# Performance work log

Hardware: AMD Instinct MI355X
Metric: run time of the kernel (lower is better)

The kernel has to match this reference:

```python
import jax, jax.numpy as jnp
import numpy as np

B, CIN, CMID, COUT, H, W = 4, 64, 128, 128, 128, 128
K = 9  # 3x3 taps
EPS = 1e-5


def conv3x3(x, w, b):
    # standard 3x3 conv, stride 1, pad 1, NCHW / OIHW
    y = jax.lax.conv_general_dilated(x, w, (1, 1), ((1, 1), (1, 1)),
                                     dimension_numbers=('NCHW', 'OIHW', 'NCHW'))
    return y + b[None, :, None, None]


def deform_conv3x3(x, offset, w, b):
    # torchvision DeformConv2d semantics (v1, no mask), kernel 3, pad 1, stride 1.
    # offset: [B, 2*K, H, W] with per-tap (dy, dx) pairs.
    Bn, C, Hn, Wn = x.shape
    off = offset.reshape(Bn, K, 2, Hn, Wn)
    off_y, off_x = off[:, :, 0], off[:, :, 1]          # [B,K,H,W]
    ky = (jnp.arange(K) // 3).astype(x.dtype)          # tap row 0..2
    kx = (jnp.arange(K) % 3).astype(x.dtype)           # tap col 0..2
    # sampling positions: p = out_pos - pad + tap + offset
    py = jnp.arange(Hn, dtype=x.dtype)[None, None, :, None] - 1.0 + ky[None, :, None, None] + off_y
    px = jnp.arange(Wn, dtype=x.dtype)[None, None, None, :] - 1.0 + kx[None, :, None, None] + off_x
    y0 = jnp.floor(py); x0 = jnp.floor(px)
    wy1 = py - y0; wx1 = px - x0                       # bilinear fractions
    y0i = y0.astype(jnp.int32); x0i = x0.astype(jnp.int32)
    xf = x.reshape(Bn, C, Hn * Wn)

    def gather(iy, ix):
        valid = ((iy >= 0) & (iy < Hn) & (ix >= 0) & (ix < Wn)).astype(x.dtype)
        idx = jnp.clip(iy, 0, Hn - 1) * Wn + jnp.clip(ix, 0, Wn - 1)  # [B,K,H,W]
        g = jax.vmap(lambda xb, ib: xb[:, ib])(xf, idx)               # [B,C,K,H,W]
        return g, valid

    g00, v00 = gather(y0i, x0i)
    g01, v01 = gather(y0i, x0i + 1)
    g10, v10 = gather(y0i + 1, x0i)
    g11, v11 = gather(y0i + 1, x0i + 1)

    def wmul(g, v, wgt):
        return g * (v * wgt)[:, None]                  # broadcast over channel dim

    sampled = (wmul(g00, v00, (1 - wy1) * (1 - wx1)) +
               wmul(g01, v01, (1 - wy1) * wx1) +
               wmul(g10, v10, wy1 * (1 - wx1)) +
               wmul(g11, v11, wy1 * wx1))              # [B,C,K,H,W]
    out = jnp.einsum('bckhw,ock->bohw', sampled, w.reshape(w.shape[0], C, K))
    return out + b[None, :, None, None]


def batchnorm_relu(x, gamma, beta):
    # training-mode BN: batch statistics over (N,H,W), biased variance
    mean = jnp.mean(x, axis=(0, 2, 3), keepdims=True)
    var = jnp.mean(jnp.square(x - mean), axis=(0, 2, 3), keepdims=True)
    y = (x - mean) * jax.lax.rsqrt(var + EPS)
    return jax.nn.relu(y * gamma[None, :, None, None] + beta[None, :, None, None])


def setup_inputs() -> dict:
    key = jax.random.key(0)
    ks = jax.random.split(key, 13)
    s = 0.05  # small weights keep offsets small / sampling mostly in-bounds
    return {
        'x': jax.random.normal(ks[0], (B, CIN, H, W), jnp.float32),
        'w_off1': jax.random.normal(ks[1], (2 * K, CIN, 3, 3), jnp.float32) * s,
        'b_off1': jnp.zeros((2 * K,), jnp.float32),
        'w1': jax.random.normal(ks[2], (CMID, CIN, 3, 3), jnp.float32) * s,
        'b1': jax.random.normal(ks[3], (CMID,), jnp.float32) * s,
        'g1': jnp.ones((CMID,), jnp.float32),
        'be1': jnp.zeros((CMID,), jnp.float32),
        'w_off2': jax.random.normal(ks[4], (2 * K, CMID, 3, 3), jnp.float32) * s,
        'b_off2': jnp.zeros((2 * K,), jnp.float32),
        'w2': jax.random.normal(ks[5], (COUT, CMID, 3, 3), jnp.float32) * s,
        'b2': jax.random.normal(ks[6], (COUT,), jnp.float32) * s,
        'g2': jnp.ones((COUT,), jnp.float32),
        'be2': jnp.zeros((COUT,), jnp.float32),
    }


def reference(x, w_off1, b_off1, w1, b1, g1, be1, w_off2, b_off2, w2, b2, g2, be2):
    offset1 = conv3x3(x, w_off1, b_off1)
    out = deform_conv3x3(x, offset1, w1, b1)
    out = batchnorm_relu(out, g1, be1)
    offset2 = conv3x3(out, w_off2, b_off2)
    out = deform_conv3x3(out, offset2, w2, b2)
    out = batchnorm_relu(out, g2, be2)
    return out
```

## Files before the change

kernel.cpp:

```cpp
#include <hip/hip_runtime.h>
#include <hip/hip_bf16.h>

#define BB 4
#define H_ 128
#define W_ 128
#define HWP 16384
#define CIN1 64
#define CMID 128
#define KOFF 18

typedef short short8 __attribute__((ext_vector_type(8)));
typedef float floatx4 __attribute__((ext_vector_type(4)));

#define WS_AB   16
#define WS_CVT  288
#define CVT_TOTAL 4447396
#define WS_WF1  4447744
#define WS_WF2  4484608
#define WS_XT   4558336
#define WS_OFF  6655488
#define WS_Y1   7835136
#define WS_Y1T  16223744
#define WS_PART 21600000
#define WS_Y2   WS_Y1

#define R_X     0
#define R_WOFF1 4194304
#define R_BOFF1 4204672
#define R_W1    4204690
#define R_B1    4278418
#define R_G1    4278546
#define R_BE1   4278674
#define R_WOFF2 4278802
#define R_BOFF2 4299538
#define R_W2    4299556
#define R_B2    4447012
#define R_G2    4447140
#define R_BE2   4447268

struct SrcPtrs { const void* p[13]; };

__device__ inline short f2bf(float f) {
    __hip_bfloat16 h = __float2bfloat16(f);
    return *reinterpret_cast<short*>(&h);
}
__device__ inline float bf2f(unsigned short u) {
    return __uint_as_float(((unsigned int)u) << 16);
}
__device__ inline float bfu_lo(unsigned int u) { return __uint_as_float(u << 16); }
__device__ inline float bfu_hi(unsigned int u) { return __uint_as_float(u & 0xFFFF0000u); }
__device__ inline float rl_f(float v, int i) {
    return __int_as_float(__builtin_amdgcn_readlane(__float_as_int(v), i));
}

__global__ void probe_dtype_k(const unsigned int* __restrict__ g1, int* __restrict__ flag) {
    if (threadIdx.x == 0 && blockIdx.x == 0) {
        flag[0] = ((g1[0] & 0xFFFFu) != 0u) ? 1 : 0;
    }
}

__global__ __launch_bounds__(256) void convert_inputs_k(SrcPtrs sp, float* __restrict__ dst,
                                                        const int* __restrict__ flag, int total) {
    int i = blockIdx.x * 256 + threadIdx.x;
    if (i >= total) return;
    constexpr int prefix[13] = {0, R_WOFF1, R_BOFF1, R_W1, R_B1, R_G1, R_BE1,
                                R_WOFF2, R_BOFF2, R_W2, R_B2, R_G2, R_BE2};
    const void* src = sp.p[0];
    int base = 0;
#pragma unroll
    for (int q = 1; q < 13; ++q) {
        if (i >= prefix[q]) { src = sp.p[q]; base = prefix[q]; }
    }
    int local = i - base;
    float v;
    if (flag[0] != 0) {
        v = bf2f(((const unsigned short*)src)[local]);
    } else {
        v = ((const float*)src)[local];
    }
    dst[i] = v;
}

template <int CIN>
__global__ __launch_bounds__(256) void wf_build_k(const float* __restrict__ w, short* __restrict__ wf) {
    constexpr int KSTEPS = CIN * 9 / 32;
    int idx = blockIdx.x * 256 + threadIdx.x;
    int j    = idx & 7;
    int lane = (idx >> 3) & 63;
    int rem  = idx >> 9;
    int ks   = rem % KSTEPS;
    int ct   = rem / KSTEPS;
    int co = ct * 16 + (lane & 15);
    int k  = ks * 32 + (lane >> 4) * 8 + j;
    int ci = k & (CIN - 1);
    int kk = k / CIN;
    wf[idx] = f2bf(w[(co * CIN + ci) * 9 + kk]);
}

__global__ __launch_bounds__(256) void xt_build_k(const float* __restrict__ x, unsigned short* __restrict__ xt) {
    __shared__ __align__(4) short s_t[64 * 66];
    int bi  = blockIdx.x;
    int hw0 = (bi & 255) * 64;
    int b   = bi >> 8;
    int t   = threadIdx.x;
    int hwp = t & 63;
#pragma unroll
    for (int it = 0; it < 16; ++it) {
        int c = it * 4 + (t >> 6);
        float v = x[((long)(b * 64 + c) << 14) + hw0 + hwp];
        s_t[hwp * 66 + c] = f2bf(v);
    }
    __syncthreads();
#pragma unroll
    for (int it = 0; it < 8; ++it) {
        int i  = it * 256 + t;
        int c2 = (i & 31) * 2;
        int hw2 = i >> 5;
        int sv = *(const int*)&s_t[hw2 * 66 + c2];
        *(int*)&xt[((long)((b << 14) + hw0 + hw2)) * 64 + c2] = sv;
    }
}

template <int CIN>
__global__ __launch_bounds__(256) void conv3x3_atomic_k(const float* __restrict__ x,
                                                        const float* __restrict__ w,
                                                        const float* __restrict__ bias,
                                                        float* __restrict__ outp) {
    constexpr int CIQ = CIN / 4;
    int bi = blockIdx.x;
    int h  = bi & 127;
    int b  = (bi >> 7) & 3;
    int q  = bi >> 9;
    int t  = threadIdx.x;
    int wq = t & 127;
    int cg = __builtin_amdgcn_readfirstlane(t >> 7);
    int co0 = cg * 9;
    int ci0 = q * CIQ;

    float acc[9];
#pragma unroll
    for (int j = 0; j < 9; ++j) acc[j] = (q == 0) ? bias[co0 + j] : 0.f;

    const float* xb = x + ((long)(b * CIN + ci0) << 14);
    bool bm = h > 0, bp = h < H_ - 1, bl = wq > 0, br = wq < W_ - 1;
    int rm = (bm ? h - 1 : 0) << 7;
    int rc = h << 7;
    int rp = (bp ? h + 1 : H_ - 1) << 7;

#pragma unroll 2
    for (int ci = 0; ci < CIQ; ++ci) {
        const float* plane = xb + ((long)ci << 14);
        float v0 = plane[rm + wq - 1], v1 = plane[rm + wq], v2 = plane[rm + wq + 1];
        float v3 = plane[rc + wq - 1], v4 = plane[rc + wq], v5 = plane[rc + wq + 1];
        float v6 = plane[rp + wq - 1], v7 = plane[rp + wq], v8 = plane[rp + wq + 1];
        v0 = (bm && bl) ? v0 : 0.f;
        v1 = bm ? v1 : 0.f;
        v2 = (bm && br) ? v2 : 0.f;
        v3 = bl ? v3 : 0.f;
        v5 = br ? v5 : 0.f;
        v6 = (bp && bl) ? v6 : 0.f;
        v7 = bp ? v7 : 0.f;
        v8 = (bp && br) ? v8 : 0.f;
#pragma unroll
        for (int j = 0; j < 9; ++j) {
            const float* wk = w + ((long)(co0 + j) * CIN + ci0 + ci) * 9;
            acc[j] += v0 * wk[0] + v1 * wk[1] + v2 * wk[2]
                    + v3 * wk[3] + v4 * wk[4] + v5 * wk[5]
                    + v6 * wk[6] + v7 * wk[7] + v8 * wk[8];
        }
    }

    long ob = ((long)(b * KOFF + co0) << 14) + (h << 7) + wq;
#pragma unroll
    for (int j = 0; j < 9; ++j) atomicAdd(&outp[ob + ((long)j << 14)], acc[j]);
}

template <int CIN>
__device__ inline void build_table(const float* __restrict__ off, int b, int h, int w0,
                                   int lane, int wv,
                                   int& tpk, float& tw0, float& tw1, float& tw2, float& tw3) {
    tpk = 0; tw0 = tw1 = tw2 = tw3 = 0.f;
    if (lane < 36) {
        int r = wv + 4 * lane;
        int p = r & 15;
        int k = r >> 4;
        int wpix = w0 + p;
        long obase = ((long)(b * KOFF) << 14) + (h << 7) + wpix;
        float oy = off[obase + ((long)(2 * k) << 14)];
        float ox = off[obase + ((long)(2 * k + 1) << 14)];
        float py = (float)(h - 1 + (k / 3)) + oy;
        float px = (float)(wpix - 1 + (k % 3)) + ox;
        float fy = floorf(py), fx = floorf(px);
        float wy = py - fy, wx = px - fx;
        int y0 = (int)fy, x0 = (int)fx;
        int y1 = y0 + 1, x1 = x0 + 1;
        bool vy0 = (y0 >= 0) && (y0 < H_);
        bool vy1 = (y1 >= 0) && (y1 < H_);
        bool vx0 = (x0 >= 0) && (x0 < W_);
        bool vx1 = (x1 >= 0) && (x1 < W_);
        float wy0 = 1.f - wy, wx0 = 1.f - wx;
        tw0 = (vy0 && vx0) ? wy0 * wx0 : 0.f;
        tw1 = (vy0 && vx1) ? wy0 * wx  : 0.f;
        tw2 = (vy1 && vx0) ? wy  * wx0 : 0.f;
        tw3 = (vy1 && vx1) ? wy  * wx  : 0.f;
        int iy0 = min(max(y0, 0), H_ - 1), iy1 = min(max(y1, 0), H_ - 1);
        int ix0 = min(max(x0, 0), W_ - 1), ix1 = min(max(x1, 0), W_ - 1);
        int dx = ix1 - ix0;
        int dy = iy1 - iy0;
        tpk = (iy0 * W_ + ix0) | (dx << 14) | (dy << 15);
    }
}

template <int NB>
__device__ inline void gather_batch128(const unsigned short* __restrict__ xb, short* __restrict__ s_samp,
                                       int PADc, int i0, int kkbase, int wv, int lane,
                                       int tpk, float tw0, float tw1, float tw2, float tw3) {
    uint4 ub[NB];
#pragma unroll
    for (int j = 0; j < NB; ++j) {
        int pk = __builtin_amdgcn_readlane(tpk, i0 + j);
        const unsigned short* b00 = xb + (pk & 0x3FFF) * 128;
        const unsigned short* b01 = b00 + ((pk >> 14) & 1) * 128;
        const unsigned short* b10 = b00 + ((pk >> 15) & 1) * (W_ * 128);
        const unsigned short* b11 = b01 + ((pk >> 15) & 1) * (W_ * 128);
        ub[j].x = *(const unsigned int*)(b00 + 2 * lane);
        ub[j].y = *(const unsigned int*)(b01 + 2 * lane);
        ub[j].z = *(const unsigned int*)(b10 + 2 * lane);
        ub[j].w = *(const unsigned int*)(b11 + 2 * lane);
    }
#pragma unroll
    for (int j = 0; j < NB; ++j) {
        int i = i0 + j;
        int r = wv + 4 * i;
        float w00 = rl_f(tw0, i), w01 = rl_f(tw1, i), w10 = rl_f(tw2, i), w11 = rl_f(tw3, i);
        float vlo = w00 * bfu_lo(ub[j].x) + w01 * bfu_lo(ub[j].y)
                  + w10 * bfu_lo(ub[j].z) + w11 * bfu_lo(ub[j].w);
        float vhi = w00 * bfu_hi(ub[j].x) + w01 * bfu_hi(ub[j].y)
                  + w10 * bfu_hi(ub[j].z) + w11 * bfu_hi(ub[j].w);
        __hip_bfloat162 h2 = __float22bfloat162_rn(make_float2(vlo, vhi));
        *(unsigned int*)&s_samp[(r & 15) * PADc + ((r >> 4) - kkbase) * 128 + 2 * lane] =
            *reinterpret_cast<unsigned int*>(&h2);
    }
}

template <int NB>
__device__ inline void gather_batch64(const unsigned short* __restrict__ xb, short* __restrict__ s_samp,
                                      int PADc, int i0, int wv, int lane,
                                      int tpk, float tw0, float tw1, float tw2, float tw3) {
    unsigned short q0[NB], q1[NB], q2[NB], q3[NB];
#pragma unroll
    for (int j = 0; j < NB; ++j) {
        int pk = __builtin_amdgcn_readlane(tpk, i0 + j);
        const unsigned short* b00 = xb + (pk & 0x3FFF) * 64;
        const unsigned short* b01 = b00 + ((pk >> 14) & 1) * 64;
        const unsigned short* b10 = b00 + ((pk >> 15) & 1) * (W_ * 64);
        const unsigned short* b11 = b01 + ((pk >> 15) & 1) * (W_ * 64);
        q0[j] = b00[lane]; q1[j] = b01[lane]; q2[j] = b10[lane]; q3[j] = b11[lane];
    }
#pragma unroll
    for (int j = 0; j < NB; ++j) {
        int i = i0 + j;
        int r = wv + 4 * i;
        float w00 = rl_f(tw0, i), w01 = rl_f(tw1, i), w10 = rl_f(tw2, i), w11 = rl_f(tw3, i);
        float v = w00 * bf2f(q0[j]) + w01 * bf2f(q1[j]) + w10 * bf2f(q2[j]) + w11 * bf2f(q3[j]);
        s_samp[(r & 15) * PADc + (r >> 4) * 64 + lane] = f2bf(v);
    }
}

__global__ __launch_bounds__(256, 6) void deform_mfma64_k(const unsigned short* __restrict__ xt,
                                                          const float* __restrict__ off,
                                                          const short* __restrict__ wf,
                                                          const float* __restrict__ bias,
                                                          float* __restrict__ out) {
    constexpr int CIN = 64;
    constexpr int K = 576;
    constexpr int PADc = K + 8;
    constexpr int KSTEPS = K / 32;
    __shared__ __align__(16) short s_samp[16 * PADc];

    int bi = blockIdx.x;
    int w0 = (bi & 7) * 16;
    int h  = (bi >> 3) & 127;
    int b  = bi >> 10;
    int t  = threadIdx.x;
    int lane = t & 63;
    int wv   = t >> 6;

    int tpk; float tw0, tw1, tw2, tw3;
    build_table<CIN>(off, b, h, w0, lane, wv, tpk, tw0, tw1, tw2, tw3);
    const unsigned short* xb = xt + (long)b * HWP * CIN;

    gather_batch64<12>(xb, s_samp, PADc,  0, wv, lane, tpk, tw0, tw1, tw2, tw3);
    gather_batch64<12>(xb, s_samp, PADc, 12, wv, lane, tpk, tw0, tw1, tw2, tw3);
    gather_batch64<12>(xb, s_samp, PADc, 24, wv, lane, tpk, tw0, tw1, tw2, tw3);
    __syncthreads();

    int p_   = lane & 15;
    int quad = lane >> 4;
    int ct0 = wv * 2, ct1 = wv * 2 + 1;
    floatx4 acc0, acc1;
#pragma unroll
    for (int r = 0; r < 4; ++r) {
        acc0[r] = bias[ct0 * 16 + quad * 4 + r];
        acc1[r] = bias[ct1 * 16 + quad * 4 + r];
    }
#pragma unroll 3
    for (int ks = 0; ks < KSTEPS; ++ks) {
        short8 bfrag = *(const short8*)&s_samp[p_ * PADc + ks * 32 + quad * 8];
        short8 a0 = *(const short8*)&wf[(((long)ct0 * KSTEPS + ks) * 64 + lane) * 8];
        short8 a1 = *(const short8*)&wf[(((long)ct1 * KSTEPS + ks) * 64 + lane) * 8];
        acc0 = __builtin_amdgcn_mfma_f32_16x16x32_bf16(a0, bfrag, acc0, 0, 0, 0);
        acc1 = __builtin_amdgcn_mfma_f32_16x16x32_bf16(a1, bfrag, acc1, 0, 0, 0);
    }

    long ob = ((long)(b * 128) << 14) + (h << 7) + w0 + p_;
#pragma unroll
    for (int r = 0; r < 4; ++r) {
        out[ob + ((long)(ct0 * 16 + quad * 4 + r) << 14)] = acc0[r];
        out[ob + ((long)(ct1 * 16 + quad * 4 + r) << 14)] = acc1[r];
    }
}

__global__ __launch_bounds__(256, 6) void deform_mfma128_k(const unsigned short* __restrict__ xt,
                                                           const float* __restrict__ off,
                                                           const short* __restrict__ wf,
                                                           const float* __restrict__ bias,
                                                           float* __restrict__ out) {
    constexpr int KSTEPS = 36;
    constexpr int PADc = 5 * 128 + 8;
    __shared__ __align__(16) short s_samp[16 * PADc];

    int bi = blockIdx.x;
    int w0 = (bi & 7) * 16;
    int h  = (bi >> 3) & 127;
    int b  = bi >> 10;
    int t  = threadIdx.x;
    int lane = t & 63;
    int wv   = t >> 6;

    int tpk; float tw0, tw1, tw2, tw3;
    build_table<128>(off, b, h, w0, lane, wv, tpk, tw0, tw1, tw2, tw3);
    const unsigned short* xb = xt + (long)b * HWP * 128;

    int p_   = lane & 15;
    int quad = lane >> 4;
    int ct0 = wv * 2, ct1 = wv * 2 + 1;
    floatx4 acc0, acc1;
#pragma unroll
    for (int r = 0; r < 4; ++r) {
        acc0[r] = bias[ct0 * 16 + quad * 4 + r];
        acc1[r] = bias[ct1 * 16 + quad * 4 + r];
    }

    gather_batch128<8>(xb, s_samp, PADc, 0, 0, wv, lane, tpk, tw0, tw1, tw2, tw3);
    gather_batch128<8>(xb, s_samp, PADc, 8, 0, wv, lane, tpk, tw0, tw1, tw2, tw3);
    __syncthreads();
#pragma unroll 4
    for (int ks = 0; ks < 16; ++ks) {
        short8 bfrag = *(const short8*)&s_samp[p_ * PADc + ks * 32 + quad * 8];
        short8 a0 = *(const short8*)&wf[(((long)ct0 * KSTEPS + ks) * 64 + lane) * 8];
        short8 a1 = *(const short8*)&wf[(((long)ct1 * KSTEPS + ks) * 64 + lane) * 8];
        acc0 = __builtin_amdgcn_mfma_f32_16x16x32_bf16(a0, bfrag, acc0, 0, 0, 0);
        acc1 = __builtin_amdgcn_mfma_f32_16x16x32_bf16(a1, bfrag, acc1, 0, 0, 0);
    }
    __syncthreads();

    gather_batch128<10>(xb, s_samp, PADc, 16, 4, wv, lane, tpk, tw0, tw1, tw2, tw3);
    gather_batch128<10>(xb, s_samp, PADc, 26, 4, wv, lane, tpk, tw0, tw1, tw2, tw3);
    __syncthreads();
#pragma unroll 4
    for (int ks = 16; ks < 36; ++ks) {
        short8 bfrag = *(const short8*)&s_samp[p_ * PADc + (ks - 16) * 32 + quad * 8];
        short8 a0 = *(const short8*)&wf[(((long)ct0 * KSTEPS + ks) * 64 + lane) * 8];
        short8 a1 = *(const short8*)&wf[(((long)ct1 * KSTEPS + ks) * 64 + lane) * 8];
        acc0 = __builtin_amdgcn_mfma_f32_16x16x32_bf16(a0, bfrag, acc0, 0, 0, 0);
        acc1 = __builtin_amdgcn_mfma_f32_16x16x32_bf16(a1, bfrag, acc1, 0, 0, 0);
    }

    long ob = ((long)(b * 128) << 14) + (h << 7) + w0 + p_;
#pragma unroll
    for (int r = 0; r < 4; ++r) {
        out[ob + ((long)(ct0 * 16 + quad * 4 + r) << 14)] = acc0[r];
        out[ob + ((long)(ct1 * 16 + quad * 4 + r) << 14)] = acc1[r];
    }
}

__global__ __launch_bounds__(256) void bn_stats_part_k(const float* __restrict__ y, float* __restrict__ part) {
    int bi = blockIdx.x;
    int c = bi & 127;
    int b = bi >> 7;
    int t = threadIdx.x;
    const float4* p4 = (const float4*)(y + ((long)(b * 128 + c) << 14));
    float sum = 0.f, ss = 0.f;
#pragma unroll
    for (int i = 0; i < 16; ++i) {
        float4 v = p4[t + 256 * i];
        sum += v.x + v.y + v.z + v.w;
        ss  += v.x * v.x + v.y * v.y + v.z * v.z + v.w * v.w;
    }
#pragma unroll
    for (int o = 32; o > 0; o >>= 1) { sum += __shfl_down(sum, o); ss += __shfl_down(ss, o); }
    __shared__ float s1[4], s2[4];
    int wave = t >> 6;
    if ((t & 63) == 0) { s1[wave] = sum; s2[wave] = ss; }
    __syncthreads();
    if (t == 0) {
        part[bi]       = s1[0] + s1[1] + s1[2] + s1[3];
        part[512 + bi] = s2[0] + s2[1] + s2[2] + s2[3];
    }
}

__global__ __launch_bounds__(256) void bn_apply_dual_k(float* __restrict__ y, const float* __restrict__ part,
                                                       const float* __restrict__ g, const float* __restrict__ be,
                                                       unsigned short* __restrict__ yt) {
    __shared__ __align__(4) short s_t[64 * 134];
    __shared__ float s_a[128], s_sh[128];
    int t = threadIdx.x;
    if (t < 128) {
        float sum = part[t] + part[128 + t] + part[256 + t] + part[384 + t];
        float ss  = part[512 + t] + part[640 + t] + part[768 + t] + part[896 + t];
        float mean = sum * (1.f / 65536.f);
        float var  = ss  * (1.f / 65536.f) - mean * mean;
        float inv  = rsqrtf(var + 1e-5f);
        float a = g[t] * inv;
        s_a[t]  = a;
        s_sh[t] = be[t] - mean * a;
    }
    __syncthreads();

    int bi  = blockIdx.x;
    int hw0 = (bi & 255) * 64;
    int b   = bi >> 8;
    int hwp = t & 63;
#pragma unroll 4
    for (int it = 0; it < 32; ++it) {
        int c = it * 4 + (t >> 6);
        float a = s_a[c], sh = s_sh[c];
        long addr = ((long)(b * 128 + c) << 14) + hw0 + hwp;
        float v = y[addr];
        v = fmaxf(v * a + sh, 0.f);
        y[addr] = v;
        s_t[hwp * 134 + c] = f2bf(v);
    }
    __syncthreads();
#pragma unroll 4
    for (int it = 0; it < 16; ++it) {
        int i   = it * 256 + t;
        int c2  = (i & 63) * 2;
        int hw2 = i >> 6;
        int sv = *(const int*)&s_t[hw2 * 134 + c2];
        *(int*)&yt[((long)((b << 14) + hw0 + hw2)) * 128 + c2] = sv;
    }
}

__global__ __launch_bounds__(256) void bn_apply_out_k(const float* __restrict__ y, const float* __restrict__ part,
                                                      const float* __restrict__ g, const float* __restrict__ be,
                                                      const int* __restrict__ flag, void* __restrict__ out, int total4) {
    __shared__ float s_a[128], s_sh[128];
    int t = threadIdx.x;
    if (t < 128) {
        float sum = part[t] + part[128 + t] + part[256 + t] + part[384 + t];
        float ss  = part[512 + t] + part[640 + t] + part[768 + t] + part[896 + t];
        float mean = sum * (1.f / 65536.f);
        float var  = ss  * (1.f / 65536.f) - mean * mean;
        float inv  = rsqrtf(var + 1e-5f);
        float a = g[t] * inv;
        s_a[t]  = a;
        s_sh[t] = be[t] - mean * a;
    }
    __syncthreads();

    int i = blockIdx.x * 256 + t;
    if (i >= total4) return;
    int c = (i >> 12) & 127;
    float a = s_a[c], sh = s_sh[c];
    float4 v = reinterpret_cast<const float4*>(y)[i];
    v.x = fmaxf(v.x * a + sh, 0.f);
    v.y = fmaxf(v.y * a + sh, 0.f);
    v.z = fmaxf(v.z * a + sh, 0.f);
    v.w = fmaxf(v.w * a + sh, 0.f);
    if (flag[0] != 0) {
        ushort4 u;
        u.x = (unsigned short)f2bf(v.x);
        u.y = (unsigned short)f2bf(v.y);
        u.z = (unsigned short)f2bf(v.z);
        u.w = (unsigned short)f2bf(v.w);
        reinterpret_cast<ushort4*>(out)[i] = u;
    } else {
        reinterpret_cast<float4*>(out)[i] = v;
    }
}

extern "C" void kernel_launch(void* const* d_in, const int* in_sizes, int n_in,
                              void* d_out, int out_size, void* d_ws, size_t ws_size,
                              hipStream_t stream) {
    float* ws   = (float*)d_ws;
    int*   flag = (int*)d_ws;
    float* cvt  = ws + WS_CVT;

    const float* X     = cvt + R_X;
    const float* Woff1 = cvt + R_WOFF1;
    const float* Boff1 = cvt + R_BOFF1;
    const float* W1f   = cvt + R_W1;
    const float* B1f   = cvt + R_B1;
    const float* G1    = cvt + R_G1;
    const float* Be1   = cvt + R_BE1;
    const float* Woff2 = cvt + R_WOFF2;
    const float* Boff2 = cvt + R_BOFF2;
    const float* W2f   = cvt + R_W2;
    const float* B2f   = cvt + R_B2;
    const float* G2    = cvt + R_G2;
    const float* Be2   = cvt + R_BE2;

    short* WF1 = (short*)(ws + WS_WF1);
    short* WF2 = (short*)(ws + WS_WF2);
    unsigned short* XT  = (unsigned short*)(ws + WS_XT);
    unsigned short* Y1T = (unsigned short*)(ws + WS_Y1T);
    float* OFF  = ws + WS_OFF;
    float* PART = ws + WS_PART;
    float* Y1   = ws + WS_Y1;
    float* Y2   = ws + WS_Y2;

    SrcPtrs sp;
    for (int j = 0; j < 13; ++j) sp.p[j] = d_in[j];

    probe_dtype_k<<<1, 64, 0, stream>>>((const unsigned int*)d_in[5], flag);
    convert_inputs_k<<<(CVT_TOTAL + 255) / 256, 256, 0, stream>>>(sp, cvt, flag, CVT_TOTAL);
    wf_build_k<64><<<288, 256, 0, stream>>>(W1f, WF1);
    wf_build_k<128><<<576, 256, 0, stream>>>(W2f, WF2);
    xt_build_k<<<1024, 256, 0, stream>>>(X, XT);

    hipMemsetAsync(OFF, 0, (size_t)KOFF * 65536 * 4, stream);
    conv3x3_atomic_k<64><<<BB * 128 * 4, 256, 0, stream>>>(X, Woff1, Boff1, OFF);
    deform_mfma64_k<<<BB * 128 * 8, 256, 0, stream>>>(XT, OFF, WF1, B1f, Y1);
    bn_stats_part_k<<<512, 256, 0, stream>>>(Y1, PART);
    bn_apply_dual_k<<<1024, 256, 0, stream>>>(Y1, PART, G1, Be1, Y1T);

    hipMemsetAsync(OFF, 0, (size_t)KOFF * 65536 * 4, stream);
    conv3x3_atomic_k<128><<<BB * 128 * 4, 256, 0, stream>>>(Y1, Woff2, Boff2, OFF);
    deform_mfma128_k<<<BB * 128 * 8, 256, 0, stream>>>(Y1T, OFF, WF2, B2f, Y2);
    bn_stats_part_k<<<512, 256, 0, stream>>>(Y2, PART);
    bn_apply_out_k<<<(BB * 128 * HWP / 4 + 255) / 256, 256, 0, stream>>>(Y2, PART, G2, Be2, flag, d_out, BB * 128 * HWP / 4);
}
```

Measured before the change: 354.0 us.

## Replace atomic offset conv with two-part split; widen deform tiles to 32 pixels

The offset conv now splits input channels into two halves that each write to their own buffer (OFF and OFFB), and the deformable kernels add the two halves together. This removes the memset and the atomic adds. The deformable MFMA kernels now use 512-thread blocks over 32-pixel tiles, with each wave owning one output-channel tile. Each weight fragment is reused for two pixel subtiles instead of loading two weight fragments per step. The 64-channel gather now uses 32-bit loads with half-wave pairing. The trade-off is a larger LDS footprint and fewer blocks per CU, and the offset conv grid has half as many blocks.

```diff
diff --git a/kernel.cpp b/kernel.cpp
--- a/kernel.cpp
+++ b/kernel.cpp
@@ -21,6 +21,7 @@
 #define WS_OFF  6655488
 #define WS_Y1   7835136
 #define WS_Y1T  16223744
+#define WS_OFFB 20418048
 #define WS_PART 21600000
 #define WS_Y2   WS_Y1
 
@@ -122,11 +123,12 @@
 }
 
 template <int CIN>
-__global__ __launch_bounds__(256) void conv3x3_atomic_k(const float* __restrict__ x,
-                                                        const float* __restrict__ w,
-                                                        const float* __restrict__ bias,
-                                                        float* __restrict__ outp) {
-    constexpr int CIQ = CIN / 4;
+__global__ __launch_bounds__(256) void conv3x3_part_k(const float* __restrict__ x,
+                                                      const float* __restrict__ w,
+                                                      const float* __restrict__ bias,
+                                                      float* __restrict__ outp,
+                                                      float* __restrict__ outpb) {
+    constexpr int CIQ = CIN / 2;
     int bi = blockIdx.x;
     int h  = bi & 127;
     int b  = (bi >> 7) & 3;
@@ -170,24 +172,26 @@
         }
     }
 
+    float* o = (q == 0) ? outp : outpb;
     long ob = ((long)(b * KOFF + co0) << 14) + (h << 7) + wq;
 #pragma unroll
-    for (int j = 0; j < 9; ++j) atomicAdd(&outp[ob + ((long)j << 14)], acc[j]);
-}
-
-template <int CIN>
-__device__ inline void build_table(const float* __restrict__ off, int b, int h, int w0,
-                                   int lane, int wv,
-                                   int& tpk, float& tw0, float& tw1, float& tw2, float& tw3) {
+    for (int j = 0; j < 9; ++j) o[ob + ((long)j << 14)] = acc[j];
+}
+
+__device__ inline void build_table2(const float* __restrict__ off, const float* __restrict__ offb,
+                                    int b, int h, int w0, int lane, int wv,
+                                    int& tpk, float& tw0, float& tw1, float& tw2, float& tw3) {
     tpk = 0; tw0 = tw1 = tw2 = tw3 = 0.f;
     if (lane < 36) {
-        int r = wv + 4 * lane;
-        int p = r & 15;
-        int k = r >> 4;
+        int r = wv + 8 * lane;
+        int p = r & 31;
+        int k = r >> 5;
         int wpix = w0 + p;
         long obase = ((long)(b * KOFF) << 14) + (h << 7) + wpix;
-        float oy = off[obase + ((long)(2 * k) << 14)];
-        float ox = off[obase + ((long)(2 * k + 1) << 14)];
+        long oyi = obase + ((long)(2 * k) << 14);
+        long oxi = obase + ((long)(2 * k + 1) << 14);
+        float oy = off[oyi] + offb[oyi];
+        float ox = off[oxi] + offb[oxi];
         float py = (float)(h - 1 + (k / 3)) + oy;
         float px = (float)(wpix - 1 + (k % 3)) + ox;
         float fy = floorf(py), fx = floorf(px);
@@ -212,9 +216,10 @@
 }
 
 template <int NB>
-__device__ inline void gather_batch128(const unsigned short* __restrict__ xb, short* __restrict__ s_samp,
-                                       int PADc, int i0, int kkbase, int wv, int lane,
-                                       int tpk, float tw0, float tw1, float tw2, float tw3) {
+__device__ inline void gather_batch128v2(const unsigned short* __restrict__ xb, short* __restrict__ s_samp,
+                                         int i0, int kkbase, int wv, int lane,
+                                         int tpk, float tw0, float tw1, float tw2, float tw3) {
+    constexpr int PADc = 648;
     uint4 ub[NB];
 #pragma unroll
     for (int j = 0; j < NB; ++j) {
@@ -231,157 +236,179 @@
 #pragma unroll
     for (int j = 0; j < NB; ++j) {
         int i = i0 + j;
-        int r = wv + 4 * i;
+        int r = wv + 8 * i;
         float w00 = rl_f(tw0, i), w01 = rl_f(tw1, i), w10 = rl_f(tw2, i), w11 = rl_f(tw3, i);
         float vlo = w00 * bfu_lo(ub[j].x) + w01 * bfu_lo(ub[j].y)
                   + w10 * bfu_lo(ub[j].z) + w11 * bfu_lo(ub[j].w);
         float vhi = w00 * bfu_hi(ub[j].x) + w01 * bfu_hi(ub[j].y)
                   + w10 * bfu_hi(ub[j].z) + w11 * bfu_hi(ub[j].w);
         __hip_bfloat162 h2 = __float22bfloat162_rn(make_float2(vlo, vhi));
-        *(unsigned int*)&s_samp[(r & 15) * PADc + ((r >> 4) - kkbase) * 128 + 2 * lane] =
+        *(unsigned int*)&s_samp[(r & 31) * PADc + ((r >> 5) - kkbase) * 128 + 2 * lane] =
             *reinterpret_cast<unsigned int*>(&h2);
     }
 }
 
-template <int NB>
-__device__ inline void gather_batch64(const unsigned short* __restrict__ xb, short* __restrict__ s_samp,
-                                      int PADc, int i0, int wv, int lane,
-                                      int tpk, float tw0, float tw1, float tw2, float tw3) {
-    unsigned short q0[NB], q1[NB], q2[NB], q3[NB];
-#pragma unroll
-    for (int j = 0; j < NB; ++j) {
-        int pk = __builtin_amdgcn_readlane(tpk, i0 + j);
+template <int NBP>
+__device__ inline void gather_batch64v2(const unsigned short* __restrict__ xb, short* __restrict__ s_samp,
+                                        int i0, int wv, int half, int li,
+                                        int tpk, float tw0, float tw1, float tw2, float tw3) {
+    constexpr int PADc = 584;
+    uint4 ub[NBP];
+#pragma unroll
+    for (int j = 0; j < NBP; ++j) {
+        int iA = i0 + 2 * j, iB = iA + 1;
+        int pkA = __builtin_amdgcn_readlane(tpk, iA);
+        int pkB = __builtin_amdgcn_readlane(tpk, iB);
+        int pk = half ? pkB : pkA;
         const unsigned short* b00 = xb + (pk & 0x3FFF) * 64;
         const unsigned short* b01 = b00 + ((pk >> 14) & 1) * 64;
         const unsigned short* b10 = b00 + ((pk >> 15) & 1) * (W_ * 64);
         const unsigned short* b11 = b01 + ((pk >> 15) & 1) * (W_ * 64);
-        q0[j] = b00[lane]; q1[j] = b01[lane]; q2[j] = b10[lane]; q3[j] = b11[lane];
-    }
-#pragma unroll
-    for (int j = 0; j < NB; ++j) {
-        int i = i0 + j;
-        int r = wv + 4 * i;
-        float w00 = rl_f(tw0, i), w01 = rl_f(tw1, i), w10 = rl_f(tw2, i), w11 = rl_f(tw3, i);
-        float v = w00 * bf2f(q0[j]) + w01 * bf2f(q1[j]) + w10 * bf2f(q2[j]) + w11 * bf2f(q3[j]);
-        s_samp[(r & 15) * PADc + (r >> 4) * 64 + lane] = f2bf(v);
-    }
-}
-
-__global__ __launch_bounds__(256, 6) void deform_mfma64_k(const unsigned short* __restrict__ xt,
+        ub[j].x = *(const unsigned int*)(b00 + 2 * li);
+        ub[j].y = *(const unsigned int*)(b01 + 2 * li);
+        ub[j].z = *(const unsigned int*)(b10 + 2 * li);
+        ub[j].w = *(const unsigned int*)(b11 + 2 * li);
+    }
+#pragma unroll
+    for (int j = 0; j < NBP; ++j) {
+        int iA = i0 + 2 * j, iB = iA + 1;
+        float w00 = half ? rl_f(tw0, iB) : rl_f(tw0, iA);
+        float w01 = half ? rl_f(tw1, iB) : rl_f(tw1, iA);
+        float w10 = half ? rl_f(tw2, iB) : rl_f(tw2, iA);
+        float w11 = half ? rl_f(tw3, iB) : rl_f(tw3, iA);
+        float vlo = w00 * bfu_lo(ub[j].x) + w01 * bfu_lo(ub[j].y)
+                  + w10 * bfu_lo(ub[j].z) + w11 * bfu_lo(ub[j].w);
+        float vhi = w00 * bfu_hi(ub[j].x) + w01 * bfu_hi(ub[j].y)
+                  + w10 * bfu_hi(ub[j].z) + w11 * bfu_hi(ub[j].w);
+        __hip_bfloat162 h2 = __float22bfloat162_rn(make_float2(vlo, vhi));
+        int r = wv + 8 * (half ? iB : iA);
+        *(unsigned int*)&s_samp[(r & 31) * PADc + (r >> 5) * 64 + 2 * li] =
+            *reinterpret_cast<unsigned int*>(&h2);
+    }
+}
+
+__global__ __launch_bounds__(512, 4) void deform_mfma64_k(const unsigned short* __restrict__ xt,
                                                           const float* __restrict__ off,
+                                                          const float* __restrict__ offb,
                                                           const short* __restrict__ wf,
                                                           const float* __restrict__ bias,
                                                           float* __restrict__ out) {
-    constexpr int CIN = 64;
-    constexpr int K = 576;
-    constexpr int PADc = K + 8;
-    constexpr int KSTEPS = K / 32;
-    __shared__ __align__(16) short s_samp[16 * PADc];
+    constexpr int KSTEPS = 18;
+    constexpr int PADc = 584;
+    __shared__ __align__(16) short s_samp[32 * PADc];
 
     int bi = blockIdx.x;
-    int w0 = (bi & 7) * 16;
-    int h  = (bi >> 3) & 127;
-    int b  = bi >> 10;
+    int w0 = (bi & 3) * 32;
+    int h  = (bi >> 2) & 127;
+    int b  = bi >> 9;
     int t  = threadIdx.x;
     int lane = t & 63;
     int wv   = t >> 6;
 
     int tpk; float tw0, tw1, tw2, tw3;
-    build_table<CIN>(off, b, h, w0, lane, wv, tpk, tw0, tw1, tw2, tw3);
-    const unsigned short* xb = xt + (long)b * HWP * CIN;
-
-    gather_batch64<12>(xb, s_samp, PADc,  0, wv, lane, tpk, tw0, tw1, tw2, tw3);
-    gather_batch64<12>(xb, s_samp, PADc, 12, wv, lane, tpk, tw0, tw1, tw2, tw3);
-    gather_batch64<12>(xb, s_samp, PADc, 24, wv, lane, tpk, tw0, tw1, tw2, tw3);
+    build_table2(off, offb, b, h, w0, lane, wv, tpk, tw0, tw1, tw2, tw3);
+    const unsigned short* xb = xt + (long)b * HWP * 64;
+    int half = lane >> 5, li = lane & 31;
+
+    gather_batch64v2<6>(xb, s_samp,  0, wv, half, li, tpk, tw0, tw1, tw2, tw3);
+    gather_batch64v2<6>(xb, s_samp, 12, wv, half, li, tpk, tw0, tw1, tw2, tw3);
+    gather_batch64v2<6>(xb, s_samp, 24, wv, half, li, tpk, tw0, tw1, tw2, tw3);
     __syncthreads();
 
     int p_   = lane & 15;
     int quad = lane >> 4;
-    int ct0 = wv * 2, ct1 = wv * 2 + 1;
+    int ct = wv;
     floatx4 acc0, acc1;
 #pragma unroll
     for (int r = 0; r < 4; ++r) {
-        acc0[r] = bias[ct0 * 16 + quad * 4 + r];
-        acc1[r] = bias[ct1 * 16 + quad * 4 + r];
+        float bv = bias[ct * 16 + quad * 4 + r];
+        acc0[r] = bv;
+        acc1[r] = bv;
     }
 #pragma unroll 3
     for (int ks = 0; ks < KSTEPS; ++ks) {
-        short8 bfrag = *(const short8*)&s_samp[p_ * PADc + ks * 32 + quad * 8];
-        short8 a0 = *(const short8*)&wf[(((long)ct0 * KSTEPS + ks) * 64 + lane) * 8];
-        short8 a1 = *(const short8*)&wf[(((long)ct1 * KSTEPS + ks) * 64 + lane) * 8];
-        acc0 = __builtin_amdgcn_mfma_f32_16x16x32_bf16(a0, bfrag, acc0, 0, 0, 0);
-        acc1 = __builtin_amdgcn_mfma_f32_16x16x32_bf16(a1, bfrag, acc1, 0, 0, 0);
+        short8 a  = *(const short8*)&wf[(((long)ct * KSTEPS + ks) * 64 + lane) * 8];
+        short8 b0 = *(const short8*)&s_samp[p_ * PADc + ks * 32 + quad * 8];
+        short8 b1 = *(const short8*)&s_samp[(16 + p_) * PADc + ks * 32 + quad * 8];
+        acc0 = __builtin_amdgcn_mfma_f32_16x16x32_bf16(a, b0, acc0, 0, 0, 0);
+        acc1 = __builtin_amdgcn_mfma_f32_16x16x32_bf16(a, b1, acc1, 0, 0, 0);
     }
 
     long ob = ((long)(b * 128) << 14) + (h << 7) + w0 + p_;
 #pragma unroll
     for (int r = 0; r < 4; ++r) {
-        out[ob + ((long)(ct0 * 16 + quad * 4 + r) << 14)] = acc0[r];
-        out[ob + ((long)(ct1 * 16 + quad * 4 + r) << 14)] = acc1[r];
-    }
-}
-
-__global__ __launch_bounds__(256, 6) void deform_mfma128_k(const unsigned short* __restrict__ xt,
+        long cpl = (long)(ct * 16 + quad * 4 + r) << 14;
+        out[ob + cpl]      = acc0[r];
+        out[ob + 16 + cpl] = acc1[r];
+    }
+}
+
+__global__ __launch_bounds__(512, 4) void deform_mfma128_k(const unsigned short* __restrict__ xt,
                                                            const float* __restrict__ off,
+                                                           const float* __restrict__ offb,
                                                            const short* __restrict__ wf,
                                                            const float* __restrict__ bias,
                                                            float* __restrict__ out) {
     constexpr int KSTEPS = 36;
-    constexpr int PADc = 5 * 128 + 8;
-    __shared__ __align__(16) short s_samp[16 * PADc];
+    constexpr int PADc = 648;
+    __shared__ __align__(16) short s_samp[32 * PADc];
 
     int bi = blockIdx.x;
-    int w0 = (bi & 7) * 16;
-    int h  = (bi >> 3) & 127;
-    int b  = bi >> 10;
+    int w0 = (bi & 3) * 32;
+    int h  = (bi >> 2) & 127;
+    int b  = bi >> 9;
     int t  = threadIdx.x;
     int lane = t & 63;
     int wv   = t >> 6;
 
     int tpk; float tw0, tw1, tw2, tw3;
-    build_table<128>(off, b, h, w0, lane, wv, tpk, tw0, tw1, tw2, tw3);
+    build_table2(off, offb, b, h, w0, lane, wv, tpk, tw0, tw1, tw2, tw3);
     const unsigned short* xb = xt + (long)b * HWP * 128;
 
     int p_   = lane & 15;
     int quad = lane >> 4;
-    int ct0 = wv * 2, ct1 = wv * 2 + 1;
+    int ct = wv;
     floatx4 acc0, acc1;
 #pragma unroll
     for (int r = 0; r < 4; ++r) {
-        acc0[r] = bias[ct0 * 16 + quad * 4 + r];
-        acc1[r] = bias[ct1 * 16 + quad * 4 + r];
-    }
-
-    gather_batch128<8>(xb, s_samp, PADc, 0, 0, wv, lane, tpk, tw0, tw1, tw2, tw3);
-    gather_batch128<8>(xb, s_samp, PADc, 8, 0, wv, lane, tpk, tw0, tw1, tw2, tw3);
+        float bv = bias[ct * 16 + quad * 4 + r];
+        acc0[r] = bv;
+        acc1[r] = bv;
+    }
+
+    gather_batch128v2<8>(xb, s_samp, 0, 0, wv, lane, tpk, tw0, tw1, tw2, tw3);
+    gather_batch128v2<8>(xb, s_samp, 8, 0, wv, lane, tpk, tw0, tw1, tw2, tw3);
     __syncthreads();
 #pragma unroll 4
     for (int ks = 0; ks < 16; ++ks) {
-        short8 bfrag = *(const short8*)&s_samp[p_ * PADc + ks * 32 + quad * 8];
-        short8 a0 = *(const short8*)&wf[(((long)ct0 * KSTEPS + ks) * 64 + lane) * 8];
-        short8 a1 = *(const short8*)&wf[(((long)ct1 * KSTEPS + ks) * 64 + lane) * 8];
-        acc0 = __builtin_amdgcn_mfma_f32_16x16x32_bf16(a0, bfrag, acc0, 0, 0, 0);
-        acc1 = __builtin_amdgcn_mfma_f32_16x16x32_bf16(a1, bfrag, acc1, 0, 0, 0);
-    }
-    __syncthreads();
-
-    gather_batch128<10>(xb, s_samp, PADc, 16, 4, wv, lane, tpk, tw0, tw1, tw2, tw3);
-    gather_batch128<10>(xb, s_samp, PADc, 26, 4, wv, lane, tpk, tw0, tw1, tw2, tw3);
+        short8 a  = *(const short8*)&wf[(((long)ct * KSTEPS + ks) * 64 + lane) * 8];
+        short8 b0 = *(const short8*)&s_samp[p_ * PADc + ks * 32 + quad * 8];
+        short8 b1 = *(const short8*)&s_samp[(16 + p_) * PADc + ks * 32 + quad * 8];
+        acc0 = __builtin_amdgcn_mfma_f32_16x16x32_bf16(a, b0, acc0, 0, 0, 0);
+        acc1 = __builtin_amdgcn_mfma_f32_16x16x32_bf16(a, b1, acc1, 0, 0, 0);
+    }
+    __syncthreads();
+
+    gather_batch128v2<5>(xb, s_samp, 16, 4, wv, lane, tpk, tw0, tw1, tw2, tw3);
+    gather_batch128v2<5>(xb, s_samp, 21, 4, wv, lane, tpk, tw0, tw1, tw2, tw3);
+    gather_batch128v2<5>(xb, s_samp, 26, 4, wv, lane, tpk, tw0, tw1, tw2, tw3);
+    gather_batch128v2<5>(xb, s_samp, 31, 4, wv, lane, tpk, tw0, tw1, tw2, tw3);
     __syncthreads();
 #pragma unroll 4
-    for (int ks = 16; ks < 36; ++ks) {
-        short8 bfrag = *(const short8*)&s_samp[p_ * PADc + (ks - 16) * 32 + quad * 8];
-        short8 a0 = *(const short8*)&wf[(((long)ct0 * KSTEPS + ks) * 64 + lane) * 8];
-        short8 a1 = *(const short8*)&wf[(((long)ct1 * KSTEPS + ks) * 64 + lane) * 8];
-        acc0 = __builtin_amdgcn_mfma_f32_16x16x32_bf16(a0, bfrag, acc0, 0, 0, 0);
-        acc1 = __builtin_amdgcn_mfma_f32_16x16x32_bf16(a1, bfrag, acc1, 0, 0, 0);
+    for (int ks = 16; ks < KSTEPS; ++ks) {
+        short8 a  = *(const short8*)&wf[(((long)ct * KSTEPS + ks) * 64 + lane) * 8];
+        short8 b0 = *(const short8*)&s_samp[p_ * PADc + (ks - 16) * 32 + quad * 8];
+        short8 b1 = *(const short8*)&s_samp[(16 + p_) * PADc + (ks - 16) * 32 + quad * 8];
+        acc0 = __builtin_amdgcn_mfma_f32_16x16x32_bf16(a, b0, acc0, 0, 0, 0);
+        acc1 = __builtin_amdgcn_mfma_f32_16x16x32_bf16(a, b1, acc1, 0, 0, 0);
     }
 
     long ob = ((long)(b * 128) << 14) + (h << 7) + w0 + p_;
 #pragma unroll
     for (int r = 0; r < 4; ++r) {
-        out[ob + ((long)(ct0 * 16 + quad * 4 + r) << 14)] = acc0[r];
-        out[ob + ((long)(ct1 * 16 + quad * 4 + r) << 14)] = acc1[r];
+        long cpl = (long)(ct * 16 + quad * 4 + r) << 14;
+        out[ob + cpl]      = acc0[r];
+        out[ob + 16 + cpl] = acc1[r];
     }
 }
 
@@ -517,6 +544,7 @@
     unsigned short* XT  = (unsigned short*)(ws + WS_XT);
     unsigned short* Y1T = (unsigned short*)(ws + WS_Y1T);
     float* OFF  = ws + WS_OFF;
+    float* OFFB = ws + WS_OFFB;
     float* PART = ws + WS_PART;
     float* Y1   = ws + WS_Y1;
     float* Y2   = ws + WS_Y2;
@@ -530,15 +558,13 @@
     wf_build_k<128><<<576, 256, 0, stream>>>(W2f, WF2);
     xt_build_k<<<1024, 256, 0, stream>>>(X, XT);
 
-    hipMemsetAsync(OFF, 0, (size_t)KOFF * 65536 * 4, stream);
-    conv3x3_atomic_k<64><<<BB * 128 * 4, 256, 0, stream>>>(X, Woff1, Boff1, OFF);
-    deform_mfma64_k<<<BB * 128 * 8, 256, 0, stream>>>(XT, OFF, WF1, B1f, Y1);
+    conv3x3_part_k<64><<<BB * 128 * 2, 256, 0, stream>>>(X, Woff1, Boff1, OFF, OFFB);
+    deform_mfma64_k<<<BB * 128 * 4, 512, 0, stream>>>(XT, OFF, OFFB, WF1, B1f, Y1);
     bn_stats_part_k<<<512, 256, 0, stream>>>(Y1, PART);
     bn_apply_dual_k<<<1024, 256, 0, stream>>>(Y1, PART, G1, Be1, Y1T);
 
-    hipMemsetAsync(OFF, 0, (size_t)KOFF * 65536 * 4, stream);
-    conv3x3_atomic_k<128><<<BB * 128 * 4, 256, 0, stream>>>(Y1, Woff2, Boff2, OFF);
-    deform_mfma128_k<<<BB * 128 * 8, 256, 0, stream>>>(Y1T, OFF, WF2, B2f, Y2);
+    conv3x3_part_k<128><<<BB * 128 * 2, 256, 0, stream>>>(Y1, Woff2, Boff2, OFF, OFFB);
+    deform_mfma128_k<<<BB * 128 * 4, 512, 0, stream>>>(Y1T, OFF, OFFB, WF2, B2f, Y2);
     bn_stats_part_k<<<512, 256, 0, stream>>>(Y2, PART);
     bn_apply_out_k<<<(BB * 128 * HWP / 4 + 255) / 256, 256, 0, stream>>>(Y2, PART, G2, Be2, flag, d_out, BB * 128 * HWP / 4);
 }
```

Result: faster. 335.2 us (-5.3%).
